# Optimization experiments

Hardware: AMD Instinct MI355X
Metric: run time of the kernel (lower is better)

## Reference

```python
import jax, jax.numpy as jnp
import numpy as np

NUM_BINS = 16
PADDING = 2.0


def _spline(u):
    # third-order (cubic B-spline) Parzen window kernel
    au = jnp.abs(u)
    su = au * au
    r1 = (4.0 - 6.0 * su + 3.0 * su * au) / 6.0          # |u| < 1
    r2 = (8.0 - 12.0 * au + 6.0 * su - su * au) / 6.0    # 1 <= |u| < 2
    return jnp.where(au < 1.0, r1, jnp.where(au < 2.0, r2, jnp.zeros_like(u)))


def setup_inputs() -> dict:
    key = jax.random.key(0)
    k1, k2 = jax.random.split(key)
    shape = (4, 1, 128, 128, 128)
    moving = jax.random.uniform(k1, shape, dtype=jnp.float32)
    fixed = jax.random.uniform(k2, shape, dtype=jnp.float32)
    return {"moving": moving, "fixed": fixed}


def reference(moving, fixed):
    nb = NUM_BINS
    B = moving.shape[0]
    m = moving.reshape(B, -1)
    f = fixed.reshape(B, -1)
    N = m.shape[1]

    fmin = f.min(1, keepdims=True); fmax = f.max(1, keepdims=True)
    mmin = m.min(1, keepdims=True); mmax = m.max(1, keepdims=True)
    fbs = (fmax - fmin) / (nb - 2.0 * PADDING)
    mbs = (mmax - mmin) / (nb - 2.0 * PADDING)

    # winTerm >= PADDING = 2, so int-truncation == floor
    f_term = f / fbs - (fmin / fbs - PADDING)
    m_term = m / mbs - (mmin / mbs - PADDING)
    f_idx = jnp.clip(f_term.astype(jnp.int32), 2, nb - 3)   # [B, N]
    m_idx = jnp.clip(m_term.astype(jnp.int32), 2, nb - 3)   # [B, N]

    b_off = jnp.arange(B, dtype=jnp.int32)[:, None]

    # joint histogram: 4-tap cubic spline scatter-add along the moving axis
    joint = jnp.zeros((B * nb * nb,), dtype=m.dtype)
    for off in (-1, 0, 1, 2):
        a = _spline((m_idx + off).astype(m_term.dtype) - m_term)  # [B, N]
        seg = (b_off * (nb * nb) + f_idx * nb + (m_idx + off)).ravel()
        joint = joint + jax.ops.segment_sum(a.ravel(), seg, num_segments=B * nb * nb)
    joint = joint.reshape(B, nb, nb)

    fixed_counts = jax.ops.segment_sum(
        jnp.ones((B * N,), dtype=m.dtype),
        (b_off * nb + f_idx).ravel(),
        num_segments=B * nb,
    ).reshape(B, nb)
    fixedPDF = fixed_counts / N                       # [B, nb]

    joint_norm = joint / joint.sum((1, 2), keepdims=True)   # [B, nb, nb]
    movingPDF = joint_norm.sum(1)                           # [B, nb]

    def plogp(p):
        return jnp.where(p > 0, p * jnp.log(jnp.where(p > 0, p, 1.0)), jnp.zeros_like(p))

    mi = plogp(joint_norm).sum((1, 2)) - plogp(movingPDF).sum(1) - plogp(fixedPDF).sum(1)
    return -jnp.mean(mi)
```

## Files before the change

kernel.cpp:

```cpp
#include <hip/hip_runtime.h>

#define NB 16
#define BATCHES 4
#define GX 128
#define BT 1024

typedef unsigned long long ull;

struct WS {
    float4 slot[BATCHES * GX];
    ull joint[BATCHES * 256];
};

__global__ __launch_bounds__(BT) void k_minmax(const float4* __restrict__ mov,
                                               const float4* __restrict__ fix,
                                               WS* __restrict__ ws, int nvec) {
    int t = threadIdx.x;
    int b = blockIdx.y, bx = blockIdx.x;
    if (bx == 0 && b == 0) ws->joint[t] = 0ull;

    const float4* m4 = mov + (size_t)b * nvec;
    const float4* f4 = fix + (size_t)b * nvec;
    int T = gridDim.x * BT;
    int i = bx * BT + t;
    float fmn = 3.4e38f, fmx = -3.4e38f, mmn = 3.4e38f, mmx = -3.4e38f;
    for (; i + 3 * T < nvec; i += 4 * T) {
        float4 f0 = f4[i], f1 = f4[i + T], f2 = f4[i + 2 * T], f3 = f4[i + 3 * T];
        float4 m0 = m4[i], m1 = m4[i + T], m2 = m4[i + 2 * T], m3 = m4[i + 3 * T];
        fmn = fminf(fmn, fminf(fminf(fminf(f0.x, f0.y), fminf(f0.z, f0.w)),
                               fminf(fminf(f1.x, f1.y), fminf(f1.z, f1.w))));
        fmn = fminf(fmn, fminf(fminf(fminf(f2.x, f2.y), fminf(f2.z, f2.w)),
                               fminf(fminf(f3.x, f3.y), fminf(f3.z, f3.w))));
        fmx = fmaxf(fmx, fmaxf(fmaxf(fmaxf(f0.x, f0.y), fmaxf(f0.z, f0.w)),
                               fmaxf(fmaxf(f1.x, f1.y), fmaxf(f1.z, f1.w))));
        fmx = fmaxf(fmx, fmaxf(fmaxf(fmaxf(f2.x, f2.y), fmaxf(f2.z, f2.w)),
                               fmaxf(fmaxf(f3.x, f3.y), fmaxf(f3.z, f3.w))));
        mmn = fminf(mmn, fminf(fminf(fminf(m0.x, m0.y), fminf(m0.z, m0.w)),
                               fminf(fminf(m1.x, m1.y), fminf(m1.z, m1.w))));
        mmn = fminf(mmn, fminf(fminf(fminf(m2.x, m2.y), fminf(m2.z, m2.w)),
                               fminf(fminf(m3.x, m3.y), fminf(m3.z, m3.w))));
        mmx = fmaxf(mmx, fmaxf(fmaxf(fmaxf(m0.x, m0.y), fmaxf(m0.z, m0.w)),
                               fmaxf(fmaxf(m1.x, m1.y), fmaxf(m1.z, m1.w))));
        mmx = fmaxf(mmx, fmaxf(fmaxf(fmaxf(m2.x, m2.y), fmaxf(m2.z, m2.w)),
                               fmaxf(fmaxf(m3.x, m3.y), fmaxf(m3.z, m3.w))));
    }
    for (; i < nvec; i += T) {
        float4 f = f4[i];
        float4 m = m4[i];
        fmn = fminf(fmn, fminf(fminf(f.x, f.y), fminf(f.z, f.w)));
        fmx = fmaxf(fmx, fmaxf(fmaxf(f.x, f.y), fmaxf(f.z, f.w)));
        mmn = fminf(mmn, fminf(fminf(m.x, m.y), fminf(m.z, m.w)));
        mmx = fmaxf(mmx, fmaxf(fmaxf(m.x, m.y), fmaxf(m.z, m.w)));
    }
    for (int d = 32; d; d >>= 1) {
        fmn = fminf(fmn, __shfl_xor(fmn, d));
        fmx = fmaxf(fmx, __shfl_xor(fmx, d));
        mmn = fminf(mmn, __shfl_xor(mmn, d));
        mmx = fmaxf(mmx, __shfl_xor(mmx, d));
    }
    __shared__ float4 wred[16];
    int wid = t >> 6, lane = t & 63;
    if (lane == 0) wred[wid] = make_float4(fmn, fmx, mmn, mmx);
    __syncthreads();
    if (wid == 0) {
        float4 s = wred[lane & 15];
        for (int d = 8; d; d >>= 1) {
            s.x = fminf(s.x, __shfl_xor(s.x, d));
            s.y = fmaxf(s.y, __shfl_xor(s.y, d));
            s.z = fminf(s.z, __shfl_xor(s.z, d));
            s.w = fmaxf(s.w, __shfl_xor(s.w, d));
        }
        if (lane == 0) ws->slot[b * GX + bx] = s;
    }
}

__global__ __launch_bounds__(BT) void k_hist(const float4* __restrict__ mov,
                                             const float4* __restrict__ fix,
                                             WS* __restrict__ ws, int nvec) {
    __shared__ ull ldsJ[16][256];
    __shared__ float4 mmbc;
    int t = threadIdx.x;
    int b = blockIdx.y, bx = blockIdx.x;
    int wid = t >> 6;

    #pragma unroll
    for (int i = 0; i < 4; i++) ((ull*)ldsJ)[t + i * BT] = 0ull;

    if (t < 64) {
        float4 a = ws->slot[b * GX + t];
        float4 c = ws->slot[b * GX + t + 64];
        float4 s = make_float4(fminf(a.x, c.x), fmaxf(a.y, c.y),
                               fminf(a.z, c.z), fmaxf(a.w, c.w));
        for (int d = 32; d; d >>= 1) {
            s.x = fminf(s.x, __shfl_xor(s.x, d));
            s.y = fmaxf(s.y, __shfl_xor(s.y, d));
            s.z = fminf(s.z, __shfl_xor(s.z, d));
            s.w = fmaxf(s.w, __shfl_xor(s.w, d));
        }
        if (t == 0) mmbc = s;
    }
    __syncthreads();

    float fbs = (mmbc.y - mmbc.x) * (1.0f / 12.0f);
    float mbs = (mmbc.w - mmbc.z) * (1.0f / 12.0f);
    float finv = 1.0f / fbs;
    float minv = 1.0f / mbs;
    float fofs = __builtin_fmaf(-mmbc.x, finv, 2.0f);
    float mofs = __builtin_fmaf(-mmbc.z, minv, 2.0f);

    ull* myJ = &ldsJ[wid][0];
    const float4* m4 = mov + (size_t)b * nvec;
    const float4* f4 = fix + (size_t)b * nvec;
    int T = gridDim.x * BT;

    auto proc = [&](float fv, float mv) {
        float fterm = __builtin_fmaf(fv, finv, fofs);
        int fi = (int)fterm;
        fi = fi < 2 ? 2 : (fi > NB - 3 ? NB - 3 : fi);
        float mterm = __builtin_fmaf(mv, minv, mofs);
        int mi_ = (int)mterm;
        mi_ = mi_ < 2 ? 2 : (mi_ > NB - 3 ? NB - 3 : mi_);
        float tt = mterm - (float)mi_;
        tt = fminf(fmaxf(tt, 0.0f), 1.0f);
        float t2 = tt * tt;
        float omt = 1.0f - tt;
        float w0 = omt * omt * omt * (1.0f / 6.0f);
        float w3 = tt * t2 * (1.0f / 6.0f);
        float w1 = __builtin_fmaf(__builtin_fmaf(3.0f, tt, -6.0f), t2, 4.0f) * (1.0f / 6.0f);
        float w2 = 1.0f - w0 - w1 - w3;
        int row = fi << 4;
        int s0 = (mi_ - 1 + 5 * fi) & 15;
        atomicAdd(myJ + row + s0,             (ull)(unsigned int)(w0 * 4294967296.0f));
        atomicAdd(myJ + row + ((s0 + 1) & 15), (ull)(unsigned int)(w1 * 4294967296.0f));
        atomicAdd(myJ + row + ((s0 + 2) & 15), (ull)(unsigned int)(w2 * 4294967296.0f));
        atomicAdd(myJ + row + ((s0 + 3) & 15), (ull)(unsigned int)(w3 * 4294967296.0f));
    };

    int i = bx * BT + t;
    for (; i + T < nvec; i += 2 * T) {
        float4 f0 = f4[i], f1 = f4[i + T];
        float4 m0 = m4[i], m1 = m4[i + T];
        proc(f0.x, m0.x); proc(f0.y, m0.y); proc(f0.z, m0.z); proc(f0.w, m0.w);
        proc(f1.x, m1.x); proc(f1.y, m1.y); proc(f1.z, m1.z); proc(f1.w, m1.w);
    }
    for (; i < nvec; i += T) {
        float4 fv = f4[i];
        float4 mv = m4[i];
        proc(fv.x, mv.x); proc(fv.y, mv.y); proc(fv.z, mv.z); proc(fv.w, mv.w);
    }
    __syncthreads();

    if (t < 256) {
        ull v = 0;
        #pragma unroll
        for (int c = 0; c < 16; c++) v += ldsJ[c][t];
        if (v) atomicAdd(&ws->joint[b * 256 + t], v);
    }
}

__global__ __launch_bounds__(256) void k_final(const WS* __restrict__ ws,
                                               float* __restrict__ out) {
    __shared__ double shp[256];
    __shared__ double wsum[4];
    int t = threadIdx.x, lane = t & 63, wid = t >> 6;
    double acc = 0.0;
    for (int b = 0; b < BATCHES; ++b) {
        ull q = ws->joint[b * 256 + t];
        double v = (double)q;
        double s = v;
        for (int d = 32; d; d >>= 1) s += __shfl_xor(s, d);
        if (lane == 0) wsum[wid] = s;
        __syncthreads();
        double total = wsum[0] + wsum[1] + wsum[2] + wsum[3];
        double p = v / total;
        int f = t >> 4, c = t & 15, m = (c - 5 * f) & 15;
        __syncthreads();
        shp[f * 16 + m] = p;
        double val = (q != 0ull) ? p * log(p) : 0.0;
        __syncthreads();
        if (t < 16) {
            double mp = 0.0;
            #pragma unroll
            for (int f2 = 0; f2 < 16; ++f2) mp += shp[f2 * 16 + t];
            if (mp > 0.0) val -= mp * log(mp);
        } else if (t < 32) {
            int f2 = t - 16;
            double fp = 0.0;
            #pragma unroll
            for (int m2 = 0; m2 < 16; ++m2) fp += shp[f2 * 16 + m2];
            if (fp > 0.0) val -= fp * log(fp);
        }
        double s2 = val;
        for (int d = 32; d; d >>= 1) s2 += __shfl_xor(s2, d);
        __syncthreads();
        if (lane == 0) wsum[wid] = s2;
        __syncthreads();
        if (t == 0) acc += wsum[0] + wsum[1] + wsum[2] + wsum[3];
        __syncthreads();
    }
    if (t == 0) out[0] = (float)(-acc / (double)BATCHES);
}

extern "C" void kernel_launch(void* const* d_in, const int* in_sizes, int n_in,
                              void* d_out, int out_size, void* d_ws, size_t ws_size,
                              hipStream_t stream) {
    const float* mov = (const float*)d_in[0];
    const float* fix = (const float*)d_in[1];
    float* out = (float*)d_out;
    WS* ws = (WS*)d_ws;

    int total = in_sizes[0];
    int N = total / BATCHES;
    int nvec = N / 4;

    dim3 grid(GX, BATCHES);
    k_minmax<<<grid, BT, 0, stream>>>((const float4*)mov, (const float4*)fix, ws, nvec);
    k_hist<<<grid, BT, 0, stream>>>((const float4*)mov, (const float4*)fix, ws, nvec);
    k_final<<<1, 256, 0, stream>>>(ws, out);
}
```

Before: 121.5 us.

## Fuse final MI reduction into histogram kernel and use 32-bit LDS atomics

Removes the separate final kernel launch by having the last histogram block, chosen through a global ticket counter, compute the entropy reduction. The per-wave LDS joint histograms switch from 64-bit to 32-bit atomics with a 2^21 fixed-point scale, which halves LDS footprint and should make the atomics cheaper. The trade-offs are lower weight precision, the ordering subtleties of the last-block pattern, and one block doing the tail work serially.

New measurement: 122.2 us. Within noise of the previous version (+0.5%).

```diff
diff --git a/kernel.cpp b/kernel.cpp
--- a/kernel.cpp
+++ b/kernel.cpp
@@ -10,6 +10,7 @@
 struct WS {
     float4 slot[BATCHES * GX];
     ull joint[BATCHES * 256];
+    unsigned int ticket;
 };
 
 __global__ __launch_bounds__(BT) void k_minmax(const float4* __restrict__ mov,
@@ -17,7 +18,10 @@
                                                WS* __restrict__ ws, int nvec) {
     int t = threadIdx.x;
     int b = blockIdx.y, bx = blockIdx.x;
-    if (bx == 0 && b == 0) ws->joint[t] = 0ull;
+    if (bx == 0 && b == 0) {
+        ws->joint[t] = 0ull;
+        if (t == 0) ws->ticket = 0u;
+    }
 
     const float4* m4 = mov + (size_t)b * nvec;
     const float4* f4 = fix + (size_t)b * nvec;
@@ -76,15 +80,19 @@
 
 __global__ __launch_bounds__(BT) void k_hist(const float4* __restrict__ mov,
                                              const float4* __restrict__ fix,
-                                             WS* __restrict__ ws, int nvec) {
-    __shared__ ull ldsJ[16][256];
+                                             WS* __restrict__ ws, int nvec,
+                                             float* __restrict__ out) {
+    __shared__ unsigned int ldsJ[16][256];
     __shared__ float4 mmbc;
+    __shared__ bool isLast;
+    __shared__ double shp[256];
+    __shared__ double wsum[4];
     int t = threadIdx.x;
     int b = blockIdx.y, bx = blockIdx.x;
     int wid = t >> 6;
 
     #pragma unroll
-    for (int i = 0; i < 4; i++) ((ull*)ldsJ)[t + i * BT] = 0ull;
+    for (int i = 0; i < 4; i++) ((unsigned int*)ldsJ)[t + i * BT] = 0u;
 
     if (t < 64) {
         float4 a = ws->slot[b * GX + t];
@@ -108,7 +116,7 @@
     float fofs = __builtin_fmaf(-mmbc.x, finv, 2.0f);
     float mofs = __builtin_fmaf(-mmbc.z, minv, 2.0f);
 
-    ull* myJ = &ldsJ[wid][0];
+    unsigned int* myJ = &ldsJ[wid][0];
     const float4* m4 = mov + (size_t)b * nvec;
     const float4* f4 = fix + (size_t)b * nvec;
     int T = gridDim.x * BT;
@@ -120,20 +128,19 @@
         float mterm = __builtin_fmaf(mv, minv, mofs);
         int mi_ = (int)mterm;
         mi_ = mi_ < 2 ? 2 : (mi_ > NB - 3 ? NB - 3 : mi_);
-        float tt = mterm - (float)mi_;
-        tt = fminf(fmaxf(tt, 0.0f), 1.0f);
+        float tt = fminf(fmaxf(mterm - (float)mi_, 0.0f), 1.0f);
         float t2 = tt * tt;
         float omt = 1.0f - tt;
         float w0 = omt * omt * omt * (1.0f / 6.0f);
         float w3 = tt * t2 * (1.0f / 6.0f);
         float w1 = __builtin_fmaf(__builtin_fmaf(3.0f, tt, -6.0f), t2, 4.0f) * (1.0f / 6.0f);
-        float w2 = 1.0f - w0 - w1 - w3;
+        float w2 = fmaxf(1.0f - w0 - w1 - w3, 0.0f);
         int row = fi << 4;
         int s0 = (mi_ - 1 + 5 * fi) & 15;
-        atomicAdd(myJ + row + s0,             (ull)(unsigned int)(w0 * 4294967296.0f));
-        atomicAdd(myJ + row + ((s0 + 1) & 15), (ull)(unsigned int)(w1 * 4294967296.0f));
-        atomicAdd(myJ + row + ((s0 + 2) & 15), (ull)(unsigned int)(w2 * 4294967296.0f));
-        atomicAdd(myJ + row + ((s0 + 3) & 15), (ull)(unsigned int)(w3 * 4294967296.0f));
+        atomicAdd(myJ + row + s0,              (unsigned int)(w0 * 2097152.0f));
+        atomicAdd(myJ + row + ((s0 + 1) & 15), (unsigned int)(w1 * 2097152.0f));
+        atomicAdd(myJ + row + ((s0 + 2) & 15), (unsigned int)(w2 * 2097152.0f));
+        atomicAdd(myJ + row + ((s0 + 3) & 15), (unsigned int)(w3 * 2097152.0f));
     };
 
     int i = bx * BT + t;
@@ -153,30 +160,35 @@
     if (t < 256) {
         ull v = 0;
         #pragma unroll
-        for (int c = 0; c < 16; c++) v += ldsJ[c][t];
+        for (int c = 0; c < 16; c++) v += (ull)ldsJ[c][t];
         if (v) atomicAdd(&ws->joint[b * 256 + t], v);
     }
-}
-
-__global__ __launch_bounds__(256) void k_final(const WS* __restrict__ ws,
-                                               float* __restrict__ out) {
-    __shared__ double shp[256];
-    __shared__ double wsum[4];
-    int t = threadIdx.x, lane = t & 63, wid = t >> 6;
+
+    if (t == 0) {
+        __threadfence();
+        unsigned int done = atomicAdd(&ws->ticket, 1u);
+        isLast = (done == (unsigned int)(gridDim.x * gridDim.y) - 1u);
+    }
+    __syncthreads();
+    if (!isLast) return;
+
     double acc = 0.0;
-    for (int b = 0; b < BATCHES; ++b) {
-        ull q = ws->joint[b * 256 + t];
-        double v = (double)q;
+    for (int bb = 0; bb < BATCHES; ++bb) {
+        double v = 0.0;
+        ull q = 0ull;
+        if (t < 256) {
+            q = atomicAdd(&ws->joint[bb * 256 + t], 0ull);
+            v = (double)q;
+        }
         double s = v;
         for (int d = 32; d; d >>= 1) s += __shfl_xor(s, d);
-        if (lane == 0) wsum[wid] = s;
+        if (t < 256 && (t & 63) == 0) wsum[t >> 6] = s;
         __syncthreads();
         double total = wsum[0] + wsum[1] + wsum[2] + wsum[3];
-        double p = v / total;
+        double p = (t < 256) ? v / total : 0.0;
         int f = t >> 4, c = t & 15, m = (c - 5 * f) & 15;
-        __syncthreads();
-        shp[f * 16 + m] = p;
-        double val = (q != 0ull) ? p * log(p) : 0.0;
+        if (t < 256) shp[f * 16 + m] = p;
+        double val = (t < 256 && q != 0ull) ? p * log(p) : 0.0;
         __syncthreads();
         if (t < 16) {
             double mp = 0.0;
@@ -193,7 +205,7 @@
         double s2 = val;
         for (int d = 32; d; d >>= 1) s2 += __shfl_xor(s2, d);
         __syncthreads();
-        if (lane == 0) wsum[wid] = s2;
+        if (t < 256 && (t & 63) == 0) wsum[t >> 6] = s2;
         __syncthreads();
         if (t == 0) acc += wsum[0] + wsum[1] + wsum[2] + wsum[3];
         __syncthreads();
@@ -215,6 +227,5 @@
 
     dim3 grid(GX, BATCHES);
     k_minmax<<<grid, BT, 0, stream>>>((const float4*)mov, (const float4*)fix, ws, nvec);
-    k_hist<<<grid, BT, 0, stream>>>((const float4*)mov, (const float4*)fix, ws, nvec);
-    k_final<<<1, 256, 0, stream>>>(ws, out);
+    k_hist<<<grid, BT, 0, stream>>>((const float4*)mov, (const float4*)fix, ws, nvec, out);
 }
```
